# Performance work log

Measured on AMD Instinct MI355X. Metric: run time of the kernel, lower is better.

The kernel has to match this reference:

```python
import jax, jax.numpy as jnp
import numpy as np
from jax.scipy.special import erf

N_POINTS = 5000
N_EVENTS = 1_000_000


def setup_inputs() -> dict:
    key = jax.random.key(0)
    k1, k2, k3, k4 = jax.random.split(key, 4)
    data_idx = jax.random.randint(k1, (N_EVENTS, 2), 0, N_POINTS, dtype=jnp.int32)
    data_t = jax.random.uniform(k2, (N_EVENTS,), dtype=jnp.float32) * 10.0
    # learned parameters, matching torch.rand(...)*0.5 init
    z0 = jax.random.uniform(k3, (N_POINTS, 2), dtype=jnp.float32) * 0.5
    v0 = jax.random.uniform(k4, (N_POINTS, 2), dtype=jnp.float32) * 0.5
    beta = jnp.ones((1, 1), dtype=jnp.float32)  # beta init = 1.0
    t0 = jnp.float32(0.0)
    tn = jnp.float32(10.0)
    return {"data_idx": data_idx, "data_t": data_t, "t0": t0, "tn": tn,
            "z0": z0, "v0": v0, "beta": beta}


def reference(data_idx, data_t, t0, tn, z0, v0, beta):
    b = beta[0, 0]
    # ---- event intensity: sum over events of (beta - ||z_i(t) - z_j(t)||^2)
    i = data_idx[:, 0]
    j = data_idx[:, 1]
    dz_e = (z0[i] - z0[j]) + (v0[i] - v0[j]) * data_t[:, None]  # [E,2]
    d_event = jnp.sum(dz_e * dz_e, axis=-1)                     # [E]
    n_events = data_t.shape[0]
    event_intensity = n_events * b - jnp.sum(d_event)

    # ---- non-event intensity: analytic integral over all node pairs i<j
    n = z0.shape[0]
    pi_idx, pj_idx = jnp.triu_indices(n, k=1)  # static node-pair list
    dz = z0[pi_idx] - z0[pj_idx]  # [P,2]
    dv = v0[pi_idx] - v0[pj_idx]  # [P,2]
    a2 = jnp.sum(dz * dz, axis=-1)       # ||dz||^2
    b2 = jnp.sum(dv * dv, axis=-1)       # ||dv||^2
    ab = jnp.sum(dz * dv, axis=-1)       # dz . dv
    bnorm = jnp.sqrt(b2)
    mu = ab / b2
    # integral_{t0}^{tn} exp(beta - ||dz + dv t||^2) dt
    #   = exp(beta - a2 + ab^2/b2) * sqrt(pi)/(2|dv|) * [erf(|dv|(tn+mu)) - erf(|dv|(t0+mu))]
    pref = jnp.exp(b - a2 + ab * mu) * (jnp.sqrt(jnp.pi) / (2.0 * bnorm))
    integral = pref * (erf(bnorm * (tn + mu)) - erf(bnorm * (t0 + mu)))
    non_event_intensity = jnp.sum(integral)

    log_likelihood = event_intensity - non_event_intensity
    return log_likelihood.reshape(1, 1)
```

## Files before the change

### kernel.cpp

```cpp
#include <hip/hip_runtime.h>
#include <math.h>

#define NTHR 256
#define MAXBLK 4096
#define PTS_PAD 20480


typedef float v2f __attribute__((ext_vector_type(2)));

__global__ void pack_kernel(const float* __restrict__ z0,
                            const float* __restrict__ v0,
                            float* __restrict__ xs, float* __restrict__ ys,
                            float* __restrict__ vxs, float* __restrict__ vys,
                            float4* __restrict__ pts, int n_pts) {
    int p = blockIdx.x * blockDim.x + threadIdx.x;
    if (p < n_pts) {
        float zx = z0[2 * p], zy = z0[2 * p + 1];
        float vx = v0[2 * p], vy = v0[2 * p + 1];
        xs[p] = zx; ys[p] = zy; vxs[p] = vx; vys[p] = vy;
        pts[p] = make_float4(zx, zy, vx, vy);
    }
}

#define ERF_A1 0.0705230784f
#define ERF_A2 0.0422820123f
#define ERF_A3 0.0092705272f
#define ERF_A4 0.0001520143f
#define ERF_A5 0.0002765672f
#define ERF_A6 0.0000430638f

__device__ __forceinline__ float erf728(float x) {
    float ax = fabsf(x);
    float h = fmaf(ERF_A6, ax, ERF_A5);
    h = fmaf(h, ax, ERF_A4);
    h = fmaf(h, ax, ERF_A3);
    h = fmaf(h, ax, ERF_A2);
    h = fmaf(h, ax, ERF_A1);
    float u = fmaf(h, ax, 1.0f);
    float w = __builtin_amdgcn_rcpf(u);
    w = w * w; w = w * w; w = w * w; w = w * w;
    return copysignf(1.0f - w, x);
}

__device__ __forceinline__ float pair_val(float4 Pi, float4 Pj,
                                          float b, float t0, float tn) {
    const float SPI2 = 0.88622692545275801365f;
    const float L2E  = 1.4426950408889634f;
    float dzx = Pi.x - Pj.x, dzy = Pi.y - Pj.y;
    float dvx = Pi.z - Pj.z, dvy = Pi.w - Pj.w;
    float a2 = fmaf(dzx, dzx, dzy * dzy);
    float b2 = fmaf(dvx, dvx, dvy * dvy);
    float ab = fmaf(dzx, dvx, dzy * dvy);
    float r  = __builtin_amdgcn_rsqf(b2);
    float mu = ab * (r * r);
    float e0 = fmaf(ab, mu, b - a2);
    float E  = __builtin_amdgcn_exp2f(e0 * L2E);
    float bn = b2 * r;
    float x1 = bn * (tn + mu);
    float x0 = bn * (t0 + mu);
    return (E * (SPI2 * r)) * (erf728(x1) - erf728(x0));
}

__device__ __forceinline__ v2f erf_u2(v2f ax) {
    v2f h = ERF_A6 * ax + ERF_A5;
    h = h * ax + ERF_A4;
    h = h * ax + ERF_A3;
    h = h * ax + ERF_A2;
    h = h * ax + ERF_A1;
    return h * ax + 1.0f;
}

__device__ __forceinline__ v2f pair_val2(float Pix, float Piy, float Pivx,
                                         float Pivy, v2f xj, v2f yj, v2f vxj,
                                         v2f vyj, float b, float t0, float tn) {
    const float SPI2 = 0.88622692545275801365f;
    const float L2E  = 1.4426950408889634f;
    v2f dzx = Pix - xj, dzy = Piy - yj;
    v2f dvx = Pivx - vxj, dvy = Pivy - vyj;
    v2f a2 = dzx * dzx + dzy * dzy;
    v2f b2 = dvx * dvx + dvy * dvy;
    v2f ab = dzx * dvx + dzy * dvy;
    v2f r;  r.x = __builtin_amdgcn_rsqf(b2.x); r.y = __builtin_amdgcn_rsqf(b2.y);
    v2f mu = ab * (r * r);
    v2f e0 = ab * mu + (b - a2);
    v2f E;  E.x = __builtin_amdgcn_exp2f(e0.x * L2E);
            E.y = __builtin_amdgcn_exp2f(e0.y * L2E);
    v2f bn = b2 * r;
    v2f x1 = bn * (tn + mu);
    v2f x0 = bn * (t0 + mu);
    v2f ax1; ax1.x = fabsf(x1.x); ax1.y = fabsf(x1.y);
    v2f ax0; ax0.x = fabsf(x0.x); ax0.y = fabsf(x0.y);
    v2f u1 = erf_u2(ax1);
    v2f u0 = erf_u2(ax0);
    v2f p = u1 * u0;
    v2f rp; rp.x = __builtin_amdgcn_rcpf(p.x); rp.y = __builtin_amdgcn_rcpf(p.y);
    v2f w1 = u0 * rp;
    v2f w0 = u1 * rp;
    w1 = w1 * w1; w1 = w1 * w1; w1 = w1 * w1; w1 = w1 * w1;
    w0 = w0 * w0; w0 = w0 * w0; w0 = w0 * w0; w0 = w0 * w0;
    v2f e1 = 1.0f - w1;
    v2f e0f = 1.0f - w0;
    e1.x = copysignf(e1.x, x1.x);  e1.y = copysignf(e1.y, x1.y);
    e0f.x = copysignf(e0f.x, x0.x); e0f.y = copysignf(e0f.y, x0.y);
    return (E * (r * SPI2)) * (e1 - e0f);
}

__device__ __forceinline__ float row_sweep(const float* __restrict__ xs,
                                           const float* __restrict__ ys,
                                           const float* __restrict__ vxs,
                                           const float* __restrict__ vys,
                                           const float4* __restrict__ pts,
                                           int r, int n_pts,
                                           float b, float t0, float tn) {
    float4 Pi = pts[r];
    float head = 0.0f;
    int base = r + 1;
    if (base & 1) {
        if (threadIdx.x == 0)
            head = pair_val(Pi, pts[base], b, t0, tn);
        ++base;
    }
    v2f acc = {0.f, 0.f};
    for (int jb = base + 2 * (int)threadIdx.x; jb < n_pts; jb += 2 * NTHR) {
        v2f xj  = *(const v2f*)(xs + jb);
        v2f yj  = *(const v2f*)(ys + jb);
        v2f vxj = *(const v2f*)(vxs + jb);
        v2f vyj = *(const v2f*)(vys + jb);
        acc += pair_val2(Pi.x, Pi.y, Pi.z, Pi.w, xj, yj, vxj, vyj, b, t0, tn);
    }
    return head + acc.x + acc.y;
}

__device__ __forceinline__ float event_sum(const int2* __restrict__ idx,
                                           const float* __restrict__ t,
                                           const float4* __restrict__ pts,
                                           int n_events, int nblocks) {
    const int4*   idx4 = (const int4*)idx;
    const float2* t2   = (const float2*)t;
    const int half = n_events >> 1;
    float acc = 0.0f;
    for (int h = blockIdx.x * NTHR + threadIdx.x; h < half;
         h += nblocks * NTHR) {
        int4 ij = idx4[h];
        float2 tt = t2[h];
        float4 pi0 = pts[ij.x], pj0 = pts[ij.y];
        float4 pi1 = pts[ij.z], pj1 = pts[ij.w];
        float dx0 = (pi0.x - pj0.x) + (pi0.z - pj0.z) * tt.x;
        float dy0 = (pi0.y - pj0.y) + (pi0.w - pj0.w) * tt.x;
        float dx1 = (pi1.x - pj1.x) + (pi1.z - pj1.z) * tt.y;
        float dy1 = (pi1.y - pj1.y) + (pi1.w - pj1.w) * tt.y;
        acc = fmaf(dx0, dx0, fmaf(dy0, dy0, acc));
        acc = fmaf(dx1, dx1, fmaf(dy1, dy1, acc));
    }
    if ((n_events & 1) && blockIdx.x == 0 && threadIdx.x == 0) {
        int e = n_events - 1;
        int2 ij = idx[e];
        float te = t[e];
        float4 pi = pts[ij.x], pj = pts[ij.y];
        float dx = (pi.x - pj.x) + (pi.z - pj.z) * te;
        float dy = (pi.y - pj.y) + (pi.w - pj.w) * te;
        acc = fmaf(dx, dx, fmaf(dy, dy, acc));
    }
    return acc;
}

__device__ __forceinline__ float pair_sum(const float* __restrict__ xs,
                                          const float* __restrict__ ys,
                                          const float* __restrict__ vxs,
                                          const float* __restrict__ vys,
                                          const float4* __restrict__ pts,
                                          int n_pts, float b, float t0,
                                          float tn) {
    const int n_rows = n_pts - 1;
    const int r1 = blockIdx.x;
    float acc = 0.0f;
    if (r1 < n_rows) {
        const int r2 = n_rows - 1 - r1;
        acc += row_sweep(xs, ys, vxs, vys, pts, r1, n_pts, b, t0, tn);
        if (r2 > r1)
            acc += row_sweep(xs, ys, vxs, vys, pts, r2, n_pts, b, t0, tn);
    }
    return acc;
}

__global__ __launch_bounds__(NTHR) void cvm_main_kernel(
    const int2* __restrict__ idx, const float* __restrict__ t,
    const float* __restrict__ xs, const float* __restrict__ ys,
    const float* __restrict__ vxs, const float* __restrict__ vys,
    const float4* __restrict__ pts,
    const float* __restrict__ t0p, const float* __restrict__ tnp,
    const float* __restrict__ betap,
    int n_events, int n_pts, double* __restrict__ partials) {

    const float b  = betap[0];
    const float t0 = t0p[0];
    const float tn = tnp[0];
    const int nblocks = gridDim.x;

    float accf;
    if (blockIdx.x & 1) {
        accf = pair_sum(xs, ys, vxs, vys, pts, n_pts, b, t0, tn);
        accf += event_sum(idx, t, pts, n_events, nblocks);
    } else {
        accf = event_sum(idx, t, pts, n_events, nblocks);
        accf += pair_sum(xs, ys, vxs, vys, pts, n_pts, b, t0, tn);
    }

    double v = (double)accf;
    #pragma unroll
    for (int off = 32; off > 0; off >>= 1) v += __shfl_down(v, off, 64);
    __shared__ double wsum[4];
    if ((threadIdx.x & 63) == 0) wsum[threadIdx.x >> 6] = v;
    __syncthreads();
    if (threadIdx.x == 0)
        partials[blockIdx.x] = wsum[0] + wsum[1] + wsum[2] + wsum[3];
}

__global__ void finish_kernel(const double* __restrict__ partials, int nblk,
                              const float* __restrict__ betap,
                              float* __restrict__ out, int n_events) {
    double v = 0.0;
    for (int i = threadIdx.x; i < nblk; i += NTHR) v += partials[i];
    #pragma unroll
    for (int off = 32; off > 0; off >>= 1) v += __shfl_down(v, off, 64);
    __shared__ double wsum[4];
    if ((threadIdx.x & 63) == 0) wsum[threadIdx.x >> 6] = v;
    __syncthreads();
    if (threadIdx.x == 0)
        out[0] = (float)((double)n_events * (double)betap[0] -
                         (wsum[0] + wsum[1] + wsum[2] + wsum[3]));
}

extern "C" void kernel_launch(void* const* d_in, const int* in_sizes, int n_in,
                              void* d_out, int out_size, void* d_ws, size_t ws_size,
                              hipStream_t stream) {
    const int2*  idx  = (const int2*)d_in[0];
    const float* t    = (const float*)d_in[1];
    const float* t0   = (const float*)d_in[2];
    const float* tn   = (const float*)d_in[3];
    const float* z0   = (const float*)d_in[4];
    const float* v0   = (const float*)d_in[5];
    const float* beta = (const float*)d_in[6];
    const int n_events = in_sizes[1];
    const int n_pts    = in_sizes[4] / 2;

    char* base = (char*)d_ws;
    double* partials = (double*)base;
    float* xs  = (float*)(base + 32768);
    float* ys  = (float*)(base + 32768 + PTS_PAD);
    float* vxs = (float*)(base + 32768 + 2 * PTS_PAD);
    float* vys = (float*)(base + 32768 + 3 * PTS_PAD);
    float4* pts = (float4*)(base + 32768 + 4 * PTS_PAD);

    const int n_rows = n_pts - 1;
    int nblk = (n_rows + 1) / 2;
    if (nblk < 1) nblk = 1;
    if (nblk > MAXBLK) nblk = MAXBLK;

    pack_kernel<<<(n_pts + NTHR - 1) / NTHR, NTHR, 0, stream>>>(
        z0, v0, xs, ys, vxs, vys, pts, n_pts);
    cvm_main_kernel<<<nblk, NTHR, 0, stream>>>(idx, t, xs, ys, vxs, vys, pts,
                                               t0, tn, beta, n_events, n_pts,
                                               partials);
    finish_kernel<<<1, NTHR, 0, stream>>>(partials, nblk, beta,
                                          (float*)d_out, n_events);
}
```

Baseline: 96.53 us.

## Fuse final reduction via last-block atomic and prefetch event loads before pair sweep

```diff
diff --git a/kernel.cpp b/kernel.cpp
--- a/kernel.cpp
+++ b/kernel.cpp
@@ -12,7 +12,8 @@
                             const float* __restrict__ v0,
                             float* __restrict__ xs, float* __restrict__ ys,
                             float* __restrict__ vxs, float* __restrict__ vys,
-                            float4* __restrict__ pts, int n_pts) {
+                            float4* __restrict__ pts,
+                            unsigned int* __restrict__ counter, int n_pts) {
     int p = blockIdx.x * blockDim.x + threadIdx.x;
     if (p < n_pts) {
         float zx = z0[2 * p], zy = z0[2 * p + 1];
@@ -20,6 +21,7 @@
         xs[p] = zx; ys[p] = zy; vxs[p] = vx; vys[p] = vy;
         pts[p] = make_float4(zx, zy, vx, vy);
     }
+    if (p == 0) *counter = 0u;
 }
 
 #define ERF_A1 0.0705230784f
@@ -131,39 +133,6 @@
     return head + acc.x + acc.y;
 }
 
-__device__ __forceinline__ float event_sum(const int2* __restrict__ idx,
-                                           const float* __restrict__ t,
-                                           const float4* __restrict__ pts,
-                                           int n_events, int nblocks) {
-    const int4*   idx4 = (const int4*)idx;
-    const float2* t2   = (const float2*)t;
-    const int half = n_events >> 1;
-    float acc = 0.0f;
-    for (int h = blockIdx.x * NTHR + threadIdx.x; h < half;
-         h += nblocks * NTHR) {
-        int4 ij = idx4[h];
-        float2 tt = t2[h];
-        float4 pi0 = pts[ij.x], pj0 = pts[ij.y];
-        float4 pi1 = pts[ij.z], pj1 = pts[ij.w];
-        float dx0 = (pi0.x - pj0.x) + (pi0.z - pj0.z) * tt.x;
-        float dy0 = (pi0.y - pj0.y) + (pi0.w - pj0.w) * tt.x;
-        float dx1 = (pi1.x - pj1.x) + (pi1.z - pj1.z) * tt.y;
-        float dy1 = (pi1.y - pj1.y) + (pi1.w - pj1.w) * tt.y;
-        acc = fmaf(dx0, dx0, fmaf(dy0, dy0, acc));
-        acc = fmaf(dx1, dx1, fmaf(dy1, dy1, acc));
-    }
-    if ((n_events & 1) && blockIdx.x == 0 && threadIdx.x == 0) {
-        int e = n_events - 1;
-        int2 ij = idx[e];
-        float te = t[e];
-        float4 pi = pts[ij.x], pj = pts[ij.y];
-        float dx = (pi.x - pj.x) + (pi.z - pj.z) * te;
-        float dy = (pi.y - pj.y) + (pi.w - pj.w) * te;
-        acc = fmaf(dx, dx, fmaf(dy, dy, acc));
-    }
-    return acc;
-}
-
 __device__ __forceinline__ float pair_sum(const float* __restrict__ xs,
                                           const float* __restrict__ ys,
                                           const float* __restrict__ vxs,
@@ -190,45 +159,88 @@
     const float4* __restrict__ pts,
     const float* __restrict__ t0p, const float* __restrict__ tnp,
     const float* __restrict__ betap,
-    int n_events, int n_pts, double* __restrict__ partials) {
+    int n_events, int n_pts,
+    double* __restrict__ partials, unsigned int* __restrict__ counter,
+    float* __restrict__ out) {
 
     const float b  = betap[0];
     const float t0 = t0p[0];
     const float tn = tnp[0];
     const int nblocks = gridDim.x;
-
-    float accf;
-    if (blockIdx.x & 1) {
-        accf = pair_sum(xs, ys, vxs, vys, pts, n_pts, b, t0, tn);
-        accf += event_sum(idx, t, pts, n_events, nblocks);
-    } else {
-        accf = event_sum(idx, t, pts, n_events, nblocks);
-        accf += pair_sum(xs, ys, vxs, vys, pts, n_pts, b, t0, tn);
+    const int tid = blockIdx.x * NTHR + (int)threadIdx.x;
+    const int nthreads = nblocks * NTHR;
+
+    const int4*   idx4 = (const int4*)idx;
+    const float2* t2   = (const float2*)t;
+    const int half = n_events >> 1;
+    const bool hasev = tid < half;
+    int4 ij; float2 tt;
+    float4 pi0, pj0, pi1, pj1;
+    if (hasev) {
+        ij = idx4[tid];
+        tt = t2[tid];
+        pi0 = pts[ij.x]; pj0 = pts[ij.y];
+        pi1 = pts[ij.z]; pj1 = pts[ij.w];
+    }
+
+    float accf = pair_sum(xs, ys, vxs, vys, pts, n_pts, b, t0, tn);
+
+    if (hasev) {
+        float dx0 = (pi0.x - pj0.x) + (pi0.z - pj0.z) * tt.x;
+        float dy0 = (pi0.y - pj0.y) + (pi0.w - pj0.w) * tt.x;
+        float dx1 = (pi1.x - pj1.x) + (pi1.z - pj1.z) * tt.y;
+        float dy1 = (pi1.y - pj1.y) + (pi1.w - pj1.w) * tt.y;
+        accf = fmaf(dx0, dx0, fmaf(dy0, dy0, accf));
+        accf = fmaf(dx1, dx1, fmaf(dy1, dy1, accf));
+    }
+    for (int h = tid + nthreads; h < half; h += nthreads) {
+        int4 ij2 = idx4[h];
+        float2 tt2 = t2[h];
+        float4 a0 = pts[ij2.x], b0 = pts[ij2.y];
+        float4 a1 = pts[ij2.z], b1 = pts[ij2.w];
+        float dx0 = (a0.x - b0.x) + (a0.z - b0.z) * tt2.x;
+        float dy0 = (a0.y - b0.y) + (a0.w - b0.w) * tt2.x;
+        float dx1 = (a1.x - b1.x) + (a1.z - b1.z) * tt2.y;
+        float dy1 = (a1.y - b1.y) + (a1.w - b1.w) * tt2.y;
+        accf = fmaf(dx0, dx0, fmaf(dy0, dy0, accf));
+        accf = fmaf(dx1, dx1, fmaf(dy1, dy1, accf));
+    }
+    if ((n_events & 1) && tid == 0) {
+        int e = n_events - 1;
+        int2 ij1 = idx[e];
+        float te = t[e];
+        float4 pi = pts[ij1.x], pj = pts[ij1.y];
+        float dx = (pi.x - pj.x) + (pi.z - pj.z) * te;
+        float dy = (pi.y - pj.y) + (pi.w - pj.w) * te;
+        accf = fmaf(dx, dx, fmaf(dy, dy, accf));
     }
 
     double v = (double)accf;
     #pragma unroll
     for (int off = 32; off > 0; off >>= 1) v += __shfl_down(v, off, 64);
     __shared__ double wsum[4];
+    __shared__ bool is_last;
     if ((threadIdx.x & 63) == 0) wsum[threadIdx.x >> 6] = v;
     __syncthreads();
-    if (threadIdx.x == 0)
+    if (threadIdx.x == 0) {
         partials[blockIdx.x] = wsum[0] + wsum[1] + wsum[2] + wsum[3];
-}
-
-__global__ void finish_kernel(const double* __restrict__ partials, int nblk,
-                              const float* __restrict__ betap,
-                              float* __restrict__ out, int n_events) {
-    double v = 0.0;
-    for (int i = threadIdx.x; i < nblk; i += NTHR) v += partials[i];
-    #pragma unroll
-    for (int off = 32; off > 0; off >>= 1) v += __shfl_down(v, off, 64);
-    __shared__ double wsum[4];
-    if ((threadIdx.x & 63) == 0) wsum[threadIdx.x >> 6] = v;
+        __threadfence();
+        unsigned int old = atomicAdd(counter, 1u);
+        is_last = (old == (unsigned int)(nblocks - 1));
+    }
     __syncthreads();
-    if (threadIdx.x == 0)
-        out[0] = (float)((double)n_events * (double)betap[0] -
-                         (wsum[0] + wsum[1] + wsum[2] + wsum[3]));
+    if (is_last) {
+        __threadfence();
+        double s = 0.0;
+        for (int i = threadIdx.x; i < nblocks; i += NTHR) s += partials[i];
+        #pragma unroll
+        for (int off = 32; off > 0; off >>= 1) s += __shfl_down(s, off, 64);
+        if ((threadIdx.x & 63) == 0) wsum[threadIdx.x >> 6] = s;
+        __syncthreads();
+        if (threadIdx.x == 0)
+            out[0] = (float)((double)n_events * (double)betap[0] -
+                             (wsum[0] + wsum[1] + wsum[2] + wsum[3]));
+    }
 }
 
 extern "C" void kernel_launch(void* const* d_in, const int* in_sizes, int n_in,
@@ -246,6 +258,7 @@
 
     char* base = (char*)d_ws;
     double* partials = (double*)base;
+    unsigned int* counter = (unsigned int*)(base + MAXBLK * sizeof(double));
     float* xs  = (float*)(base + 32768);
     float* ys  = (float*)(base + 32768 + PTS_PAD);
     float* vxs = (float*)(base + 32768 + 2 * PTS_PAD);
@@ -258,10 +271,8 @@
     if (nblk > MAXBLK) nblk = MAXBLK;
 
     pack_kernel<<<(n_pts + NTHR - 1) / NTHR, NTHR, 0, stream>>>(
-        z0, v0, xs, ys, vxs, vys, pts, n_pts);
+        z0, v0, xs, ys, vxs, vys, pts, counter, n_pts);
     cvm_main_kernel<<<nblk, NTHR, 0, stream>>>(idx, t, xs, ys, vxs, vys, pts,
                                                t0, tn, beta, n_events, n_pts,
-                                               partials);
-    finish_kernel<<<1, NTHR, 0, stream>>>(partials, nblk, beta,
-                                          (float*)d_out, n_events);
-}
+                                               partials, counter, (float*)d_out);
+}
```

Result: slower. 136.0 us (+40.9%).
